# Optimization experiments

Hardware: AMD Instinct MI355X
Metric: run time of the kernel (lower is better)

Reference implementation:

```python
import jax, jax.numpy as jnp
import numpy as np

NU = 100000  # num 'user' nodes
NI = 100000  # num 'item' nodes
E = 600000   # edges per relation
IN_DIM = 128
HID = 128
OUT = 64


def setup_inputs() -> dict:
    key = jax.random.key(0)
    ks = jax.random.split(key, 14)
    return {
        "x_user": jax.random.normal(ks[0], (NU, IN_DIM), jnp.float32),
        "x_item": jax.random.normal(ks[1], (NI, IN_DIM), jnp.float32),
        "W_proj": jax.random.normal(ks[2], (IN_DIM, HID), jnp.float32) / np.sqrt(IN_DIM),
        "b_proj": jax.random.normal(ks[3], (HID,), jnp.float32) * 0.01,
        "W_out": jax.random.normal(ks[4], (HID, OUT), jnp.float32) / np.sqrt(HID),
        "b_out": jax.random.normal(ks[5], (OUT,), jnp.float32) * 0.01,
        "al1": jax.random.normal(ks[6], (1,), jnp.float32),
        "ar1": jax.random.normal(ks[7], (1,), jnp.float32),
        "al2": jax.random.normal(ks[8], (1,), jnp.float32),
        "ar2": jax.random.normal(ks[9], (1,), jnp.float32),
        "e1_src": jax.random.randint(ks[10], (E,), 0, NU, jnp.int32),  # user->user
        "e1_dst": jax.random.randint(ks[11], (E,), 0, NU, jnp.int32),
        "e2_src": jax.random.randint(ks[12], (E,), 0, NI, jnp.int32),  # item->user
        "e2_dst": jax.random.randint(ks[13], (E,), 0, NU, jnp.int32),
    }


def reference(x_user, x_item, W_proj, b_proj, W_out, b_out,
              al1, ar1, al2, ar2, e1_src, e1_dst, e2_src, e2_dst):
    # Shared projection for every node type
    h_user = x_user @ W_proj + b_proj  # [NU, HID]
    h_item = x_item @ W_proj + b_proj  # [NI, HID]

    # Relation ('user','u2u','user'): msg = h_src*al + h_dst*ar, scatter-add to dst
    msg1 = h_user[e1_src] * al1 + h_user[e1_dst] * ar1  # [E, HID]
    out_user = jax.ops.segment_sum(msg1, e1_dst, num_segments=NU)

    # Relation ('item','i2u','user')
    msg2 = h_item[e2_src] * al2 + h_user[e2_dst] * ar2  # [E, HID]
    out_user = out_user + jax.ops.segment_sum(msg2, e2_dst, num_segments=NU)

    # 'item' receives no messages -> zeros
    out_item = jnp.zeros_like(h_item)

    out_user = jax.nn.elu(out_user)
    out_item = jax.nn.elu(out_item)

    # out_layer applied only to 'user'
    out_user = out_user @ W_out + b_out  # [NU, OUT]
    return out_user, out_item
```

## Files before the change

kernel.cpp:

```cpp
#include <hip/hip_runtime.h>
#include <hip/hip_bf16.h>
#include <math.h>

#define NUSER 100000
#define NITEM 100000
#define NEDGE 600000
#define HID   128
#define OUTD  64
#define LDA   136
#define LDF   132
#define BLKR  128
#define PROJ_BLOCKS ((NUSER + NITEM + BLKR - 1) / BLKR)
#define EPB   ((2 * NEDGE + PROJ_BLOCKS - 1) / PROJ_BLOCKS)

typedef __attribute__((ext_vector_type(8))) short  bf16x8;
typedef __attribute__((ext_vector_type(4))) float  f32x4;
typedef __attribute__((ext_vector_type(4))) unsigned short u16x4;

__device__ inline unsigned short f2bf(float f) {
    __hip_bfloat16 h = __float2bfloat16(f);
    return *reinterpret_cast<unsigned short*>(&h);
}

__device__ inline void bf2x(unsigned int u, float& lo, float& hi) {
    union { unsigned int i; float f; } a, b;
    a.i = u << 16;
    b.i = u & 0xffff0000u;
    lo = a.f; hi = b.f;
}

__global__ void prep(const float* __restrict__ W, unsigned short* __restrict__ wt,
                     int* __restrict__ deg) {
    int i = blockIdx.x * 256 + threadIdx.x;
    if (i < 2 * NUSER) deg[i] = 0;
    if (i < 128 * 128) {
        int k = i >> 7, c = i & 127;
        wt[c * 128 + k] = f2bf(W[i]);
    }
}

__device__ inline void cr_one(int i, const int* e1d, const int* e2d,
                              int* deg1, int* deg2, int* rank) {
    if (i < NEDGE)            rank[i] = atomicAdd(&deg1[e1d[i]], 1);
    else if (i < 2 * NEDGE)   rank[i] = atomicAdd(&deg2[e2d[i - NEDGE]], 1);
}

__global__ void count_rank(const int* __restrict__ e1d, const int* __restrict__ e2d,
                           int* __restrict__ deg1, int* __restrict__ deg2,
                           int* __restrict__ rank) {
    int i0 = blockIdx.x * 512 + threadIdx.x;
    cr_one(i0, e1d, e2d, deg1, deg2, rank);
    cr_one(i0 + 256, e1d, e2d, deg1, deg2, rank);
}

#define SCAN_BLOCKS 391

__global__ __launch_bounds__(256) void scanA(
    const int* __restrict__ deg1, const int* __restrict__ deg2,
    int* __restrict__ off, int* __restrict__ bsum)
{
    __shared__ int sh[256];
    int t = threadIdx.x;
    int i = blockIdx.x * 256 + t;
    int d = (i < NUSER) ? deg1[i] + deg2[i] : 0;
    sh[t] = d;
    __syncthreads();
    for (int dd = 1; dd < 256; dd <<= 1) {
        int v = (t >= dd) ? sh[t - dd] : 0;
        __syncthreads();
        sh[t] += v;
        __syncthreads();
    }
    if (i < NUSER) off[i] = (t > 0) ? sh[t - 1] : 0;
    if (t == 255) bsum[blockIdx.x] = sh[255];
}

__global__ __launch_bounds__(512) void scanB(int* __restrict__ bsum, int* __restrict__ off) {
    __shared__ int sh[512];
    int t = threadIdx.x;
    int v = (t < SCAN_BLOCKS) ? bsum[t] : 0;
    sh[t] = v;
    __syncthreads();
    for (int dd = 1; dd < 512; dd <<= 1) {
        int x = (t >= dd) ? sh[t - dd] : 0;
        __syncthreads();
        sh[t] += x;
        __syncthreads();
    }
    if (t < SCAN_BLOCKS) bsum[t] = (t > 0) ? sh[t - 1] : 0;
    if (t == 511) off[NUSER] = sh[511];
}

__global__ __launch_bounds__(256) void scanC(int* __restrict__ off, const int* __restrict__ bsum) {
    int i = blockIdx.x * 256 + threadIdx.x;
    if (i < NUSER) off[i] += bsum[blockIdx.x];
}

__global__ __launch_bounds__(256) void proj_fill(
    const float* __restrict__ xu, const float* __restrict__ xi,
    const unsigned short* __restrict__ wt, const float* __restrict__ b,
    unsigned short* __restrict__ h,
    const int* __restrict__ e1s, const int* __restrict__ e1d,
    const int* __restrict__ e2s, const int* __restrict__ e2d,
    const int* __restrict__ off, const int* __restrict__ deg1,
    const int* __restrict__ rank, int* __restrict__ adj)
{
    __shared__ unsigned short Al[BLKR * LDA];
    const int tid = threadIdx.x;
    const int r0  = blockIdx.x * BLKR;

    #pragma unroll
    for (int half = 0; half < 2; half++) {
        float4 v[8];
        #pragma unroll
        for (int j = 0; j < 8; j++) {
            int i = tid + (half * 8 + j) * 256;
            int row = i >> 5, c4 = i & 31;
            int gr = r0 + row;
            const float* srcp;
            if (gr < NUSER) srcp = xu + (size_t)gr * 128;
            else {
                int g2 = gr - NUSER;
                if (g2 > NITEM - 1) g2 = NITEM - 1;
                srcp = xi + (size_t)g2 * 128;
            }
            v[j] = ((const float4*)srcp)[c4];
        }
        __builtin_amdgcn_sched_barrier(0);
        #pragma unroll
        for (int j = 0; j < 8; j++) {
            int i = tid + (half * 8 + j) * 256;
            int row = i >> 5, c4 = i & 31;
            u16x4 p;
            p.x = f2bf(v[j].x); p.y = f2bf(v[j].y); p.z = f2bf(v[j].z); p.w = f2bf(v[j].w);
            *(u16x4*)&Al[row * LDA + c4 * 4] = p;
        }
    }
    __syncthreads();

    const int w    = tid >> 6;
    const int lane = tid & 63;
    const int lrow = lane & 15;
    const int lk   = (lane >> 4) * 8;

    bf16x8 bfrag[4][2];
    #pragma unroll
    for (int kc = 0; kc < 4; kc++) {
        const int ko = kc * 32 + lk;
        bfrag[kc][0] = *(const bf16x8*)&wt[(size_t)(w * 32 + lrow) * 128 + ko];
        bfrag[kc][1] = *(const bf16x8*)&wt[(size_t)(w * 32 + 16 + lrow) * 128 + ko];
    }

    f32x4 acc[8][2] = {};
    #pragma unroll
    for (int kc = 0; kc < 4; kc++) {
        const int ko = kc * 32 + lk;
        #pragma unroll
        for (int rt = 0; rt < 8; rt++) {
            bf16x8 aa = *(const bf16x8*)&Al[(rt * 16 + lrow) * LDA + ko];
            acc[rt][0] = __builtin_amdgcn_mfma_f32_16x16x32_bf16(aa, bfrag[kc][0], acc[rt][0], 0, 0, 0);
            acc[rt][1] = __builtin_amdgcn_mfma_f32_16x16x32_bf16(aa, bfrag[kc][1], acc[rt][1], 0, 0, 0);
        }
    }

    __syncthreads();
    const float bv0 = b[w * 32 + lrow];
    const float bv1 = b[w * 32 + 16 + lrow];
    #pragma unroll
    for (int rt = 0; rt < 8; rt++) {
        #pragma unroll
        for (int ct = 0; ct < 2; ct++) {
            int col = w * 32 + ct * 16 + lrow;
            float bv = ct ? bv1 : bv0;
            #pragma unroll
            for (int r = 0; r < 4; r++) {
                int row = rt * 16 + (lane >> 4) * 4 + r;
                Al[row * LDA + col] = f2bf(acc[rt][ct][r] + bv);
            }
        }
    }
    __syncthreads();

    #pragma unroll
    for (int j = 0; j < 8; j++) {
        int i = tid + j * 256;
        int row = i >> 4, c8 = i & 15;
        int gr = r0 + row;
        if (gr < NUSER + NITEM)
            *(bf16x8*)&h[(size_t)gr * 128 + c8 * 8] =
                *(const bf16x8*)&Al[row * LDA + c8 * 8];
    }

    const int base = blockIdx.x * EPB;
    #pragma unroll
    for (int t = 0; t < 3; t++) {
        int i = base + tid + t * 256;
        if (i >= 2 * NEDGE) continue;
        int src, dst, slot;
        if (i < NEDGE) {
            src  = e1s[i];
            dst  = e1d[i];
            slot = off[dst] + rank[i];
        } else {
            int j = i - NEDGE;
            src  = NUSER + e2s[j];
            dst  = e2d[j];
            slot = off[dst] + deg1[dst] + rank[i];
        }
        adj[slot] = src;
    }
}

__global__ __launch_bounds__(256) void gather(
    const unsigned short* __restrict__ h, const int* __restrict__ adj,
    const int* __restrict__ off, const int* __restrict__ deg1,
    const int* __restrict__ deg2,
    const float* __restrict__ al1p, const float* __restrict__ ar1p,
    const float* __restrict__ al2p, const float* __restrict__ ar2p,
    unsigned int* __restrict__ accb)
{
    int wv   = (int)((blockIdx.x * 256 + threadIdx.x) >> 6);
    int lane = threadIdx.x & 63;
    if (wv >= NUSER / 2) return;
    const int nA = 2 * wv, nB = 2 * wv + 1;

    const unsigned int* h32 = (const unsigned int*)h;
    const float al1 = al1p[0], al2 = al2p[0];
    const float ar1 = ar1p[0], ar2 = ar2p[0];

    int offA = off[nA], offM = off[nA + 1], offE = off[nA + 2];
    const float scA = ar1 * (float)deg1[nA] + ar2 * (float)deg2[nA];
    const float scB = ar1 * (float)deg1[nB] + ar2 * (float)deg2[nB];

    float xA, yA, xB, yB;
    bf2x(h32[(size_t)nA * 64 + lane], xA, yA);
    bf2x(h32[(size_t)nB * 64 + lane], xB, yB);
    float sxA = scA * xA, syA = scA * yA;
    float sxB = scB * xB, syB = scB * yB;

    int eA = offA, endA = offM;
    int eB = offM, endB = offE;

    while (eA + 4 <= endA && eB + 4 <= endB) {
        int sA[4], sB[4];
        #pragma unroll
        for (int j = 0; j < 4; j++) { sA[j] = adj[eA + j]; sB[j] = adj[eB + j]; }
        unsigned int uA[4], uB[4];
        #pragma unroll
        for (int j = 0; j < 4; j++) {
            uA[j] = h32[(size_t)sA[j] * 64 + lane];
            uB[j] = h32[(size_t)sB[j] * 64 + lane];
        }
        #pragma unroll
        for (int j = 0; j < 4; j++) {
            float a = (sA[j] < NUSER) ? al1 : al2;
            float x, y; bf2x(uA[j], x, y);
            sxA = fmaf(a, x, sxA); syA = fmaf(a, y, syA);
            float b2 = (sB[j] < NUSER) ? al1 : al2;
            bf2x(uB[j], x, y);
            sxB = fmaf(b2, x, sxB); syB = fmaf(b2, y, syB);
        }
        eA += 4; eB += 4;
    }
    while (eA + 4 <= endA) {
        int s[4];
        #pragma unroll
        for (int j = 0; j < 4; j++) s[j] = adj[eA + j];
        unsigned int u[4];
        #pragma unroll
        for (int j = 0; j < 4; j++) u[j] = h32[(size_t)s[j] * 64 + lane];
        #pragma unroll
        for (int j = 0; j < 4; j++) {
            float a = (s[j] < NUSER) ? al1 : al2;
            float x, y; bf2x(u[j], x, y);
            sxA = fmaf(a, x, sxA); syA = fmaf(a, y, syA);
        }
        eA += 4;
    }
    for (; eA < endA; eA++) {
        int s0 = adj[eA];
        float a = (s0 < NUSER) ? al1 : al2;
        float x, y; bf2x(h32[(size_t)s0 * 64 + lane], x, y);
        sxA = fmaf(a, x, sxA); syA = fmaf(a, y, syA);
    }
    while (eB + 4 <= endB) {
        int s[4];
        #pragma unroll
        for (int j = 0; j < 4; j++) s[j] = adj[eB + j];
        unsigned int u[4];
        #pragma unroll
        for (int j = 0; j < 4; j++) u[j] = h32[(size_t)s[j] * 64 + lane];
        #pragma unroll
        for (int j = 0; j < 4; j++) {
            float a = (s[j] < NUSER) ? al1 : al2;
            float x, y; bf2x(u[j], x, y);
            sxB = fmaf(a, x, sxB); syB = fmaf(a, y, syB);
        }
        eB += 4;
    }
    for (; eB < endB; eB++) {
        int s0 = adj[eB];
        float a = (s0 < NUSER) ? al1 : al2;
        float x, y; bf2x(h32[(size_t)s0 * 64 + lane], x, y);
        sxB = fmaf(a, x, sxB); syB = fmaf(a, y, syB);
    }

    sxA = sxA > 0.f ? sxA : expm1f(sxA);
    syA = syA > 0.f ? syA : expm1f(syA);
    sxB = sxB > 0.f ? sxB : expm1f(sxB);
    syB = syB > 0.f ? syB : expm1f(syB);
    accb[(size_t)nA * 64 + lane] = ((unsigned int)f2bf(syA) << 16) | (unsigned int)f2bf(sxA);
    accb[(size_t)nB * 64 + lane] = ((unsigned int)f2bf(syB) << 16) | (unsigned int)f2bf(sxB);
}

__global__ __launch_bounds__(256) void finalize(
    const unsigned int* __restrict__ accb, const float* __restrict__ Wo,
    const float* __restrict__ bo, float* __restrict__ out)
{
    __shared__ float Wl[128 * 64];
    __shared__ float Al[64 * LDF];
    const int tid = threadIdx.x;
    const int n0  = blockIdx.x * 64;

    for (int i = tid; i < 128 * 64 / 4; i += 256)
        ((float4*)Wl)[i] = ((const float4*)Wo)[i];

    for (int i = tid; i < 4096; i += 256) {
        int row = i >> 6, d = i & 63;
        int gr = n0 + row;
        float lo = 0.f, hi = 0.f;
        if (gr < NUSER) bf2x(accb[(size_t)gr * 64 + d], lo, hi);
        *(float2*)&Al[row * LDF + d * 2] = make_float2(lo, hi);
    }
    __syncthreads();

    const int tr = tid >> 4;
    const int tc = tid & 15;

    float s[4][4];
    {
        float4 bv = *(const float4*)&bo[tc * 4];
        #pragma unroll
        for (int i = 0; i < 4; i++) {
            s[i][0] = bv.x; s[i][1] = bv.y; s[i][2] = bv.z; s[i][3] = bv.w;
        }
    }

    for (int k0 = 0; k0 < 128; k0 += 4) {
        float4 av[4];
        #pragma unroll
        for (int i = 0; i < 4; i++)
            av[i] = *(const float4*)&Al[(tr * 4 + i) * LDF + k0];
        #pragma unroll
        for (int kk = 0; kk < 4; kk++) {
            float4 wv = *(const float4*)&Wl[(k0 + kk) * 64 + tc * 4];
            #pragma unroll
            for (int i = 0; i < 4; i++) {
                float a = (&av[i].x)[kk];
                s[i][0] = fmaf(a, wv.x, s[i][0]);
                s[i][1] = fmaf(a, wv.y, s[i][1]);
                s[i][2] = fmaf(a, wv.z, s[i][2]);
                s[i][3] = fmaf(a, wv.w, s[i][3]);
            }
        }
    }

    #pragma unroll
    for (int i = 0; i < 4; i++) {
        int gr = n0 + tr * 4 + i;
        if (gr < NUSER) {
            float4 o = make_float4(s[i][0], s[i][1], s[i][2], s[i][3]);
            *(float4*)&out[(size_t)gr * 64 + tc * 4] = o;
        }
    }
}

extern "C" void kernel_launch(void* const* d_in, const int* in_sizes, int n_in,
                              void* d_out, int out_size, void* d_ws, size_t ws_size,
                              hipStream_t stream) {
    const float* xu  = (const float*)d_in[0];
    const float* xi  = (const float*)d_in[1];
    const float* Wp  = (const float*)d_in[2];
    const float* bp  = (const float*)d_in[3];
    const float* Wo  = (const float*)d_in[4];
    const float* bo  = (const float*)d_in[5];
    const float* al1 = (const float*)d_in[6];
    const float* ar1 = (const float*)d_in[7];
    const float* al2 = (const float*)d_in[8];
    const float* ar2 = (const float*)d_in[9];
    const int* e1s = (const int*)d_in[10];
    const int* e1d = (const int*)d_in[11];
    const int* e2s = (const int*)d_in[12];
    const int* e2d = (const int*)d_in[13];

    float* out   = (float*)d_out;
    float* oitem = out + (size_t)NUSER * OUTD;

    unsigned short* h    = (unsigned short*)d_ws;
    unsigned short* wt   = h + (size_t)(NUSER + NITEM) * HID;
    unsigned int*   accb = (unsigned int*)(wt + 128 * 128);

    int* meta = (int*)out;
    int* deg1 = meta;
    int* deg2 = meta + NUSER;
    int* off  = meta + 2 * NUSER;
    int* bsum = meta + 3 * NUSER + 64;
    int* adj  = meta + 3 * NUSER + 1024;
    int* rank = adj + 2 * NEDGE;

    hipMemsetAsync(oitem, 0, (size_t)NITEM * HID * sizeof(float), stream);

    prep<<<(2 * NUSER + 255) / 256, 256, 0, stream>>>(Wp, wt, deg1);

    count_rank<<<(2 * NEDGE + 511) / 512, 256, 0, stream>>>(e1d, e2d, deg1, deg2, rank);

    scanA<<<SCAN_BLOCKS, 256, 0, stream>>>(deg1, deg2, off, bsum);
    scanB<<<1, 512, 0, stream>>>(bsum, off);
    scanC<<<SCAN_BLOCKS, 256, 0, stream>>>(off, bsum);

    proj_fill<<<PROJ_BLOCKS, 256, 0, stream>>>(xu, xi, wt, bp, h,
                                               e1s, e1d, e2s, e2d,
                                               off, deg1, rank, adj);

    gather<<<(NUSER / 2 * 64) / 256, 256, 0, stream>>>(h, adj, off, deg1, deg2,
                                                       al1, ar1, al2, ar2, accb);

    finalize<<<(NUSER + 63) / 64, 256, 0, stream>>>(accb, Wo, bo, out);
}
```

Measured before the change: 232.0 us.

## Shrink projection tiles, prefetch edge-fill loads early, fold item zeroing into gather

The projection/adjacency-fill kernel now handles 32 rows per block instead of 128, giving four times as many smaller blocks with less shared memory and fewer accumulators each. Each thread loads its single edge's src/dst/rank, and the off/deg1 lookup, before the MFMA work, so that gather latency overlaps the projection. The separate memset of the zero item output is removed and done inside the gather kernel instead, saving one launch. In exchange, each block reloads the W fragments for less work, and the exact-division block counts drop the bounds checks.

```diff
diff --git a/kernel.cpp b/kernel.cpp
--- a/kernel.cpp
+++ b/kernel.cpp
@@ -9,9 +9,9 @@
 #define OUTD  64
 #define LDA   136
 #define LDF   132
-#define BLKR  128
-#define PROJ_BLOCKS ((NUSER + NITEM + BLKR - 1) / BLKR)
-#define EPB   ((2 * NEDGE + PROJ_BLOCKS - 1) / PROJ_BLOCKS)
+#define BLKR  32
+#define PROJ_BLOCKS ((NUSER + NITEM) / BLKR)
+#define EPB   ((2 * NEDGE) / PROJ_BLOCKS)
 
 typedef __attribute__((ext_vector_type(8))) short  bf16x8;
 typedef __attribute__((ext_vector_type(4))) float  f32x4;
@@ -109,32 +109,41 @@
     const int tid = threadIdx.x;
     const int r0  = blockIdx.x * BLKR;
 
-    #pragma unroll
-    for (int half = 0; half < 2; half++) {
-        float4 v[8];
-        #pragma unroll
-        for (int j = 0; j < 8; j++) {
-            int i = tid + (half * 8 + j) * 256;
-            int row = i >> 5, c4 = i & 31;
-            int gr = r0 + row;
-            const float* srcp;
-            if (gr < NUSER) srcp = xu + (size_t)gr * 128;
-            else {
-                int g2 = gr - NUSER;
-                if (g2 > NITEM - 1) g2 = NITEM - 1;
-                srcp = xi + (size_t)g2 * 128;
-            }
-            v[j] = ((const float4*)srcp)[c4];
-        }
-        __builtin_amdgcn_sched_barrier(0);
-        #pragma unroll
-        for (int j = 0; j < 8; j++) {
-            int i = tid + (half * 8 + j) * 256;
-            int row = i >> 5, c4 = i & 31;
-            u16x4 p;
-            p.x = f2bf(v[j].x); p.y = f2bf(v[j].y); p.z = f2bf(v[j].z); p.w = f2bf(v[j].w);
-            *(u16x4*)&Al[row * LDA + c4 * 4] = p;
-        }
+    int fsrc = 0, fdst = -1, frank = 0, frel2 = 0;
+    if (tid < EPB) {
+        int i = blockIdx.x * EPB + tid;
+        if (i < NEDGE) {
+            fsrc = e1s[i];  fdst = e1d[i];  frank = rank[i];
+        } else {
+            int j = i - NEDGE;
+            fsrc = NUSER + e2s[j];  fdst = e2d[j];  frank = rank[i];  frel2 = 1;
+        }
+    }
+
+    float4 v[4];
+    #pragma unroll
+    for (int j = 0; j < 4; j++) {
+        int i = tid + j * 256;
+        int row = i >> 5, c4 = i & 31;
+        int gr = r0 + row;
+        const float* srcp = (gr < NUSER) ? xu + (size_t)gr * 128
+                                         : xi + (size_t)(gr - NUSER) * 128;
+        v[j] = ((const float4*)srcp)[c4];
+    }
+    __builtin_amdgcn_sched_barrier(0);
+    #pragma unroll
+    for (int j = 0; j < 4; j++) {
+        int i = tid + j * 256;
+        int row = i >> 5, c4 = i & 31;
+        u16x4 p;
+        p.x = f2bf(v[j].x); p.y = f2bf(v[j].y); p.z = f2bf(v[j].z); p.w = f2bf(v[j].w);
+        *(u16x4*)&Al[row * LDA + c4 * 4] = p;
+    }
+
+    int foff = 0, fd1 = 0;
+    if (fdst >= 0) {
+        foff = off[fdst];
+        if (frel2) fd1 = deg1[fdst];
     }
     __syncthreads();
 
@@ -151,12 +160,12 @@
         bfrag[kc][1] = *(const bf16x8*)&wt[(size_t)(w * 32 + 16 + lrow) * 128 + ko];
     }
 
-    f32x4 acc[8][2] = {};
+    f32x4 acc[2][2] = {};
     #pragma unroll
     for (int kc = 0; kc < 4; kc++) {
         const int ko = kc * 32 + lk;
         #pragma unroll
-        for (int rt = 0; rt < 8; rt++) {
+        for (int rt = 0; rt < 2; rt++) {
             bf16x8 aa = *(const bf16x8*)&Al[(rt * 16 + lrow) * LDA + ko];
             acc[rt][0] = __builtin_amdgcn_mfma_f32_16x16x32_bf16(aa, bfrag[kc][0], acc[rt][0], 0, 0, 0);
             acc[rt][1] = __builtin_amdgcn_mfma_f32_16x16x32_bf16(aa, bfrag[kc][1], acc[rt][1], 0, 0, 0);
@@ -167,7 +176,7 @@
     const float bv0 = b[w * 32 + lrow];
     const float bv1 = b[w * 32 + 16 + lrow];
     #pragma unroll
-    for (int rt = 0; rt < 8; rt++) {
+    for (int rt = 0; rt < 2; rt++) {
         #pragma unroll
         for (int ct = 0; ct < 2; ct++) {
             int col = w * 32 + ct * 16 + lrow;
@@ -182,33 +191,15 @@
     __syncthreads();
 
     #pragma unroll
-    for (int j = 0; j < 8; j++) {
+    for (int j = 0; j < 2; j++) {
         int i = tid + j * 256;
         int row = i >> 4, c8 = i & 15;
-        int gr = r0 + row;
-        if (gr < NUSER + NITEM)
-            *(bf16x8*)&h[(size_t)gr * 128 + c8 * 8] =
-                *(const bf16x8*)&Al[row * LDA + c8 * 8];
-    }
-
-    const int base = blockIdx.x * EPB;
-    #pragma unroll
-    for (int t = 0; t < 3; t++) {
-        int i = base + tid + t * 256;
-        if (i >= 2 * NEDGE) continue;
-        int src, dst, slot;
-        if (i < NEDGE) {
-            src  = e1s[i];
-            dst  = e1d[i];
-            slot = off[dst] + rank[i];
-        } else {
-            int j = i - NEDGE;
-            src  = NUSER + e2s[j];
-            dst  = e2d[j];
-            slot = off[dst] + deg1[dst] + rank[i];
-        }
-        adj[slot] = src;
-    }
+        *(bf16x8*)&h[(size_t)(r0 + row) * 128 + c8 * 8] =
+            *(const bf16x8*)&Al[row * LDA + c8 * 8];
+    }
+
+    if (fdst >= 0)
+        adj[foff + fd1 + frank] = fsrc;
 }
 
 __global__ __launch_bounds__(256) void gather(
@@ -217,8 +208,13 @@
     const int* __restrict__ deg2,
     const float* __restrict__ al1p, const float* __restrict__ ar1p,
     const float* __restrict__ al2p, const float* __restrict__ ar2p,
-    unsigned int* __restrict__ accb)
+    unsigned int* __restrict__ accb, float* __restrict__ oitem)
 {
+    {
+        size_t zi = (size_t)blockIdx.x * 256 + threadIdx.x;
+        ((float4*)oitem)[zi] = make_float4(0.f, 0.f, 0.f, 0.f);
+    }
+
     int wv   = (int)((blockIdx.x * 256 + threadIdx.x) >> 6);
     int lane = threadIdx.x & 63;
     if (wv >= NUSER / 2) return;
@@ -408,8 +404,6 @@
     int* adj  = meta + 3 * NUSER + 1024;
     int* rank = adj + 2 * NEDGE;
 
-    hipMemsetAsync(oitem, 0, (size_t)NITEM * HID * sizeof(float), stream);
-
     prep<<<(2 * NUSER + 255) / 256, 256, 0, stream>>>(Wp, wt, deg1);
 
     count_rank<<<(2 * NEDGE + 511) / 512, 256, 0, stream>>>(e1d, e2d, deg1, deg2, rank);
@@ -423,7 +417,7 @@
                                                off, deg1, rank, adj);
 
     gather<<<(NUSER / 2 * 64) / 256, 256, 0, stream>>>(h, adj, off, deg1, deg2,
-                                                       al1, ar1, al2, ar2, accb);
+                                                       al1, ar1, al2, ar2, accb, oitem);
 
     finalize<<<(NUSER + 63) / 64, 256, 0, stream>>>(accb, Wo, bo, out);
 }
```

New measurement: 229.6 us. Within noise of the previous version (-1.1%).
